# Optimization experiments

Hardware: AMD Instinct MI355X
Metric: run time of the kernel (lower is better)

## Reference

```python
import jax, jax.numpy as jnp
import numpy as np

DIM = 128
HEADS = 8
DIM_HEAD = 128  # must equal DIM for the module's shapes to be consistent
INNER = HEADS * DIM_HEAD  # 1024
B, N = 16, 2048
SCALE = 1.0 / (DIM // 2 + 1)  # 1/65


def setup_inputs() -> dict:
    key = jax.random.key(0)
    k1, k2, k3 = jax.random.split(key, 3)
    x = jax.random.normal(k1, (B, N, DIM), dtype=jnp.float32)
    w_qkv = jax.random.normal(k2, (DIM, 3 * INNER), dtype=jnp.float32) * (DIM ** -0.5)
    w_out = jax.random.normal(k3, (INNER, DIM), dtype=jnp.float32) * (INNER ** -0.5)
    b_out = jnp.zeros((DIM,), dtype=jnp.float32)
    return {"x": x, "w_qkv": w_qkv, "w_out": w_out, "b_out": b_out}


def reference(x, w_qkv, w_out, b_out):
    b, n, dim = x.shape
    qkv = x @ w_qkv                                   # [b, n, 3*inner]
    q, k, v = jnp.split(qkv, 3, axis=-1)
    # b n (h d) -> b h n d
    to_heads = lambda t: t.reshape(b, n, HEADS, DIM_HEAD).transpose(0, 2, 1, 3)
    q, k, v = to_heads(q), to_heads(k), to_heads(v)
    xq_ft = jnp.abs(jnp.fft.rfft(q * SCALE, axis=-1))  # [b, h, n, f] real
    xk_ft = jnp.abs(jnp.fft.rfft(k * SCALE, axis=-1))
    xv_ft = jnp.fft.rfft(v, axis=-1)                   # complex
    att = jnp.einsum('bhex,bhey->bhxy', xq_ft, xk_ft)  # [b, h, f, f]
    att = jax.nn.softmax(att, axis=-1)
    xqkv_ft = jnp.einsum('bhxy,bhey->bhex', att.astype(xv_ft.dtype), xv_ft)
    out = jnp.fft.irfft(xqkv_ft, n=dim, axis=-1)       # [b, h, n, dim]
    out = out.transpose(0, 2, 1, 3).reshape(b, n, HEADS * dim)  # b n (h d)
    return out @ w_out + b_out
```

## Files before the change

kernel.cpp:

```cpp
#include <hip/hip_runtime.h>
#include <hip/hip_bf16.h>
#include <math.h>

#define NB    16
#define NSEQ  2048
#define MROWS (NB*NSEQ)

typedef __attribute__((ext_vector_type(8))) short bf16x8;
typedef __attribute__((ext_vector_type(4))) float f32x4;

__device__ __forceinline__ void g2l16(const void* g, void* l) {
    __builtin_amdgcn_global_load_lds(
        (const __attribute__((address_space(1))) void*)g,
        (__attribute__((address_space(3))) void*)l, 16, 0, 0);
}

__device__ __forceinline__ ushort f2bfu(float x) {
    __hip_bfloat16 t = __float2bfloat16(x);
    return *reinterpret_cast<ushort*>(&t);
}

__global__ __launch_bounds__(256) void k_misc(const float* __restrict__ x,
                                              const float* __restrict__ wqkv,
                                              const float* __restrict__ wout,
                                              __hip_bfloat16* __restrict__ Xb,
                                              ushort* __restrict__ Wvb,
                                              ushort* __restrict__ Wqkb,
                                              ushort* __restrict__ Gcat,
                                              ushort* __restrict__ Fcs,
                                              ushort* __restrict__ Bas) {
    __shared__ float tc[128], ts[128];
    int tid = threadIdx.x;
    int bid = blockIdx.x;
    if (bid < 4096) {
        int i = bid * 256 + tid;
        float4 v = ((const float4*)x)[i];
        __hip_bfloat16 o[4] = {__float2bfloat16(v.x), __float2bfloat16(v.y),
                               __float2bfloat16(v.z), __float2bfloat16(v.w)};
        *(ushort4*)((ushort*)Xb + (size_t)i * 4) = *(const ushort4*)o;
    } else if (bid < 4224) {
        int u = bid - 4096;
        float4 v = *(const float4*)(wqkv + (size_t)u * 3072 + 2048 + tid * 4);
        ushort o[4] = {f2bfu(v.x), f2bfu(v.y), f2bfu(v.z), f2bfu(v.w)};
        *(ushort4*)(Wvb + (size_t)u * 1024 + tid * 4) = *(const ushort4*)o;
    } else if (bid < 4352) {
        int u = bid - 4224;
        #pragma unroll
        for (int it = 0; it < 2; ++it) {
            int i = it * 256 + tid;
            float4 v = ((const float4*)(wqkv + (size_t)u * 3072))[i];
            ushort o[4] = {f2bfu(v.x), f2bfu(v.y), f2bfu(v.z), f2bfu(v.w)};
            *(ushort4*)(Wqkb + (size_t)u * 2048 + i * 4) = *(const ushort4*)o;
        }
    } else if (bid < 4872) {
        int hx = bid - 4352;
        if (tid < 128) {
            float a = (float)tid / 64.0f;
            tc[tid] = cospif(a);
            ts[tid] = sinpif(a);
        }
        __syncthreads();
        if (tid < 128) {
            int h = hx / 65, xx = hx - h * 65;
            float w = (xx == 0 || xx == 64) ? (1.0f / 128.0f) : (2.0f / 128.0f);
            float ar = 0.f, ai = 0.f;
            #pragma unroll 8
            for (int d = 0; d < 128; ++d) {
                float wv = wout[(size_t)(h * 128 + d) * 128 + tid];
                int m = (xx * d) & 127;
                ar = fmaf(wv, tc[m], ar);
                ai = fmaf(wv, ts[m], ai);
            }
            ushort* gp = Gcat + ((size_t)(h * 128 + tid)) * 160;
            gp[xx] = f2bfu(ar * w);
            gp[80 + xx] = f2bfu(-ai * w);
            if (xx == 0) {
                for (int k = 65; k < 80; ++k) gp[k] = 0;
                for (int k = 145; k < 160; ++k) gp[k] = 0;
            }
        }
    } else if (bid < 4888) {
        int r = (bid - 4872) * 16 + (tid >> 4);
        int d = r & 127;
        int y0 = (tid & 15) * 6;
        #pragma unroll
        for (int k = 0; k < 6; ++k) {
            int y = y0 + k;
            float v = 0.f;
            if (y < 65) {
                float a = (float)((d * y) & 127) / 64.0f;
                v = (r < 128) ? cospif(a) : -sinpif(a);
            }
            Fcs[r * 96 + y] = f2bfu(v);
        }
    } else {
        int idx = bid - 4888;
        int rj = idx * 16 + (tid >> 4);
        int ri = (rj >= 80) ? 1 : 0;
        int f = rj - ri * 80;
        int d0 = (tid & 15) * 8;
        #pragma unroll
        for (int k = 0; k < 8; ++k) {
            int d = d0 + k;
            float a = (float)((f * d) & 127) / 64.0f;
            float v = (ri ? -sinpif(a) : cospif(a)) * (1.0f / 65.0f);
            Bas[rj * 128 + d] = f2bfu(v);
        }
    }
}

__global__ __launch_bounds__(256) void k_wfold(const ushort* __restrict__ Wqkb,
                                               const ushort* __restrict__ Bas,
                                               ushort* __restrict__ Wt2) {
    __shared__ ushort As[128 * 128];
    __shared__ ushort Bs[160 * 128];
    int tid = threadIdx.x;
    int wave = tid >> 6, lane = tid & 63;
    int reg = blockIdx.x >> 3, h = blockIdx.x & 7;
    const ushort* ga = Wqkb + reg * 1024 + h * 128;
    #pragma unroll
    for (int it = 0; it < 8; ++it) {
        int q0 = wave * 512 + it * 64;
        int q = q0 + lane;
        int row = q >> 4, cp = q & 15;
        int gc = cp ^ (row & 15);
        g2l16(ga + (size_t)row * 2048 + gc * 8, As + q0 * 8);
    }
    #pragma unroll
    for (int it = 0; it < 10; ++it) {
        int q0 = it * 256 + wave * 64;
        int q = q0 + lane;
        int row = q >> 4, cp = q & 15;
        int gc = cp ^ (row & 15);
        g2l16(Bas + (size_t)row * 128 + gc * 8, Bs + q0 * 8);
    }
    __syncthreads();

    f32x4 acc[4][5];
    #pragma unroll
    for (int i = 0; i < 4; ++i)
        #pragma unroll
        for (int j = 0; j < 5; ++j) acc[i][j] = (f32x4){0.f, 0.f, 0.f, 0.f};

    int lr = lane & 15, lk = lane >> 4;
    int wr = (wave >> 1) * 64;
    int wn = (wave & 1) * 80;
    #pragma unroll
    for (int kk = 0; kk < 4; ++kk) {
        bf16x8 af[4], bfr[5];
        int c = kk * 4 + lk;
        #pragma unroll
        for (int i = 0; i < 4; ++i) {
            int m = wr + i * 16 + lr;
            af[i] = *(const bf16x8*)(As + m * 128 + (c ^ (m & 15)) * 8);
        }
        #pragma unroll
        for (int j = 0; j < 5; ++j) {
            int n = wn + j * 16 + lr;
            bfr[j] = *(const bf16x8*)(Bs + n * 128 + (c ^ (n & 15)) * 8);
        }
        #pragma unroll
        for (int i = 0; i < 4; ++i)
            #pragma unroll
            for (int j = 0; j < 5; ++j)
                acc[i][j] = __builtin_amdgcn_mfma_f32_16x16x32_bf16(af[i], bfr[j], acc[i][j], 0, 0, 0);
    }

    #pragma unroll
    for (int j = 0; j < 5; ++j) {
        int rj = wn + j * 16 + lr;
        int n = (h * 2 + reg) * 160 + rj;
        #pragma unroll
        for (int i = 0; i < 4; ++i) {
            int c0 = wr + i * 16 + lk * 4;
            union { ushort4 u4; ushort u[4]; } pk;
            #pragma unroll
            for (int r = 0; r < 4; ++r) pk.u[r] = f2bfu(acc[i][j][r]);
            *(ushort4*)(Wt2 + (size_t)n * 128 + c0) = pk.u4;
        }
    }
}

__global__ __launch_bounds__(320, 3) void k_fuse(const __hip_bfloat16* __restrict__ Xb,
                                                 const ushort* __restrict__ Wt2,
                                                 float* __restrict__ attp) {
    __shared__ ushort As[128 * 128];
    __shared__ ushort S[160 * 128];
    int tid = threadIdx.x;
    int wave = tid >> 6, lane = tid & 63;
    int lr = lane & 15, lk = lane >> 4;
    int lin = blockIdx.y * 128 + blockIdx.x;
    int nl = (lin & 7) * 64 + (lin >> 3);
    int b = nl >> 5;
    int epart = (nl >> 3) & 3, h = nl & 7;
    size_t erow0 = (size_t)b * NSEQ + (size_t)epart * 512;
    const ushort* wh = Wt2 + (size_t)h * 320 * 128;

    bf16x8 bw[4][4];
    #pragma unroll
    for (int ks = 0; ks < 4; ++ks)
        #pragma unroll
        for (int rb = 0; rb < 4; ++rb) {
            int n = rb * 80 + wave * 16 + lr;
            bw[ks][rb] = *(const bf16x8*)(wh + (size_t)n * 128 + (ks * 4 + lk) * 8);
        }

    {
        const ushort* gx = (const ushort*)Xb + erow0 * 128;
        for (int r = wave; r < 32; r += 5) {
            int q0 = r * 64, q = q0 + lane;
            int row = q >> 4, cp = q & 15;
            int gc = cp ^ (row & 15);
            g2l16(gx + (size_t)row * 128 + gc * 8, As + q0 * 8);
        }
    }
    __syncthreads();

    f32x4 acc2[5];
    #pragma unroll
    for (int j = 0; j < 5; ++j) acc2[j] = (f32x4){0.f, 0.f, 0.f, 0.f};

    for (int it = 0; it < 4; ++it) {
        #pragma unroll
        for (int et = 0; et < 8; ++et) {
            f32x4 a4[4];
            #pragma unroll
            for (int rb = 0; rb < 4; ++rb) a4[rb] = (f32x4){0.f, 0.f, 0.f, 0.f};
            #pragma unroll
            for (int ks = 0; ks < 4; ++ks) {
                int m = et * 16 + lr;
                bf16x8 xa = *(const bf16x8*)(As + m * 128 + (((ks * 4 + lk) ^ (m & 15))) * 8);
                #pragma unroll
                for (int rb = 0; rb < 4; ++rb)
                    a4[rb] = __builtin_amdgcn_mfma_f32_16x16x32_bf16(xa, bw[ks][rb], a4[rb], 0, 0, 0);
            }
            int e4 = et * 16 + lk * 4;
            int cq = e4 >> 3, sub = e4 & 7;
            union { ushort4 u4; ushort u[4]; } pq, pk2;
            #pragma unroll
            for (int r = 0; r < 4; ++r) {
                pq.u[r]  = f2bfu(__builtin_amdgcn_sqrtf(a4[0][r] * a4[0][r] + a4[1][r] * a4[1][r]));
                pk2.u[r] = f2bfu(__builtin_amdgcn_sqrtf(a4[2][r] * a4[2][r] + a4[3][r] * a4[3][r]));
            }
            int fq = wave * 16 + lr;
            int fk = 80 + wave * 16 + lr;
            *(ushort4*)(S + fq * 128 + ((cq ^ (fq & 15)) << 3) + sub) = pq.u4;
            *(ushort4*)(S + fk * 128 + ((cq ^ (fk & 15)) << 3) + sub) = pk2.u4;
        }
        __syncthreads();
        if (it < 3) {
            const ushort* gx = (const ushort*)Xb + (erow0 + (size_t)(it + 1) * 128) * 128;
            for (int r = wave; r < 32; r += 5) {
                int q0 = r * 64, q = q0 + lane;
                int row = q >> 4, cp = q & 15;
                int gc = cp ^ (row & 15);
                g2l16(gx + (size_t)row * 128 + gc * 8, As + q0 * 8);
            }
        }
        #pragma unroll
        for (int ks = 0; ks < 4; ++ks) {
            int cg = ks * 4 + lk;
            int xr = wave * 16 + lr;
            bf16x8 qa = *(const bf16x8*)(S + xr * 128 + ((cg ^ (xr & 15)) << 3));
            #pragma unroll
            for (int kt = 0; kt < 5; ++kt) {
                int yr = 80 + kt * 16 + lr;
                bf16x8 kb = *(const bf16x8*)(S + yr * 128 + ((cg ^ (yr & 15)) << 3));
                acc2[kt] = __builtin_amdgcn_mfma_f32_16x16x32_bf16(qa, kb, acc2[kt], 0, 0, 0);
            }
        }
        __syncthreads();
    }

    float* outp = attp + ((size_t)(b * 8 + h) * 4 + epart) * 6400;
    #pragma unroll
    for (int kt = 0; kt < 5; ++kt)
        #pragma unroll
        for (int r = 0; r < 4; ++r)
            outp[(wave * 16 + lk * 4 + r) * 80 + kt * 16 + lr] = acc2[kt][r];
}

__global__ void k_softmax(const float* __restrict__ attp, ushort* __restrict__ AttB) {
    int xx = blockIdx.x;
    int bh = blockIdx.y;
    int lane = threadIdx.x;
    ushort* Ab = AttB + (size_t)bh * 8320;
    if (xx >= 65) {
        Ab[xx * 104 + lane] = 0;
        if (lane < 40) Ab[xx * 104 + 64 + lane] = 0;
        return;
    }
    const float* base = attp + (size_t)bh * 4 * 6400 + xx * 80;
    float v0 = 0.f, v1 = 0.f;
    #pragma unroll
    for (int c = 0; c < 4; ++c) {
        v0 += base[(size_t)c * 6400 + lane];
        if (lane == 0) v1 += base[(size_t)c * 6400 + 64];
    }
    float v1b = __shfl(v1, 0);
    float m = fmaxf(v0, v1b);
    #pragma unroll
    for (int off = 32; off >= 1; off >>= 1) m = fmaxf(m, __shfl_xor(m, off));
    float e0 = expf(v0 - m);
    float e1 = expf(v1b - m);
    float s = e0;
    #pragma unroll
    for (int off = 32; off >= 1; off >>= 1) s += __shfl_xor(s, off);
    s += e1;
    float inv = 1.0f / s;
    Ab[xx * 104 + lane] = f2bfu(e0 * inv);
    if (lane == 0) Ab[xx * 104 + 64] = f2bfu(e1 * inv);
    if (lane < 39) Ab[xx * 104 + 65 + lane] = 0;
}

__global__ __launch_bounds__(256) void k_TP(const ushort* __restrict__ AttB,
                                            const ushort* __restrict__ Fcs,
                                            const ushort* __restrict__ Gcat,
                                            ushort* __restrict__ Pt) {
    __shared__ ushort A3[128 * 168];
    int tid = threadIdx.x;
    int wave = tid >> 6, lane = tid & 63;
    int lr = lane & 15, quad = lane >> 4;
    int chalf = blockIdx.x, bh = blockIdx.y;
    int b = bh >> 3, h = bh & 7;

    uint2 z2; z2.x = 0; z2.y = 0;
    uint2* A3v = (uint2*)A3;
    #pragma unroll 4
    for (int i = tid; i < 128 * 168 / 4; i += 256) A3v[i] = z2;
    __syncthreads();
    const ushort* Ab = AttB + (size_t)bh * 8320;

    f32x4 acc1[4][5];
    #pragma unroll
    for (int i = 0; i < 4; ++i)
        #pragma unroll
        for (int j = 0; j < 5; ++j) acc1[i][j] = (f32x4){0.f, 0.f, 0.f, 0.f};
    #pragma unroll
    for (int ks = 0; ks < 3; ++ks) {
        bf16x8 af[4], bfr[5];
        #pragma unroll
        for (int mi = 0; mi < 4; ++mi)
            af[mi] = *(const bf16x8*)(Fcs + (size_t)((wave * 4 + mi) * 16 + lr) * 96 + ks * 32 + quad * 8);
        #pragma unroll
        for (int nt = 0; nt < 5; ++nt)
            bfr[nt] = *(const bf16x8*)(Ab + (nt * 16 + lr) * 104 + ks * 32 + quad * 8);
        #pragma unroll
        for (int mi = 0; mi < 4; ++mi)
            #pragma unroll
            for (int nt = 0; nt < 5; ++nt)
                acc1[mi][nt] = __builtin_amdgcn_mfma_f32_16x16x32_bf16(af[mi], bfr[nt], acc1[mi][nt], 0, 0, 0);
    }
    #pragma unroll
    for (int nt = 0; nt < 5; ++nt) {
        int x = nt * 16 + lr;
        if (x < 65) {
            #pragma unroll
            for (int mi = 0; mi < 4; ++mi) {
                int wbase = (wave * 4 + mi) * 16 + quad * 4;
                #pragma unroll
                for (int r = 0; r < 4; ++r) {
                    int which = wbase + r;
                    int d = which & 127;
                    int kc = (which >> 7) * 80 + x;
                    A3[d * 168 + kc] = f2bfu(acc1[mi][nt][r]);
                }
            }
        }
    }
    __syncthreads();

    f32x4 acc2[2][4];
    #pragma unroll
    for (int i = 0; i < 2; ++i)
        #pragma unroll
        for (int j = 0; j < 4; ++j) acc2[i][j] = (f32x4){0.f, 0.f, 0.f, 0.f};
    const ushort* Gh = Gcat + (size_t)h * 128 * 160;
    #pragma unroll
    for (int ks = 0; ks < 5; ++ks) {
        bf16x8 a2[2], b2[4];
        #pragma unroll
        for (int mi = 0; mi < 2; ++mi)
            a2[mi] = *(const bf16x8*)(A3 + ((wave * 2 + mi) * 16 + lr) * 168 + ks * 32 + quad * 8);
        #pragma unroll
        for (int nt = 0; nt < 4; ++nt)
            b2[nt] = *(const bf16x8*)(Gh + (size_t)(chalf * 64 + nt * 16 + lr) * 160 + ks * 32 + quad * 8);
        #pragma unroll
        for (int mi = 0; mi < 2; ++mi)
            #pragma unroll
            for (int nt = 0; nt < 4; ++nt)
                acc2[mi][nt] = __builtin_amdgcn_mfma_f32_16x16x32_bf16(a2[mi], b2[nt], acc2[mi][nt], 0, 0, 0);
    }
    #pragma unroll
    for (int mi = 0; mi < 2; ++mi) {
        int dbase = (wave * 2 + mi) * 16 + quad * 4;
        #pragma unroll
        for (int nt = 0; nt < 4; ++nt) {
            int c = chalf * 64 + nt * 16 + lr;
            union { ushort4 u4; ushort u[4]; } pk;
            #pragma unroll
            for (int r = 0; r < 4; ++r) pk.u[r] = f2bfu(acc2[mi][nt][r]);
            *(ushort4*)(Pt + ((size_t)(b * 128 + c)) * 1024 + h * 128 + dbase) = pk.u4;
        }
    }
}

__global__ __launch_bounds__(256) void k_R(const ushort* __restrict__ Wvb,
                                           const ushort* __restrict__ Pt,
                                           ushort* __restrict__ Rt) {
    __shared__ ushort As[128 * 128];
    __shared__ ushort Bs[128 * 128];
    int tid = threadIdx.x;
    int wave = tid >> 6, lane = tid & 63;
    int b = blockIdx.x;
    const ushort* pb = Pt + (size_t)b * 128 * 1024;

    f32x4 acc[4][4];
    #pragma unroll
    for (int i = 0; i < 4; ++i)
        #pragma unroll
        for (int j = 0; j < 4; ++j) acc[i][j] = (f32x4){0.f, 0.f, 0.f, 0.f};

    int lr = lane & 15, lk = lane >> 4;
    int wr = (wave >> 1) * 64, wc = (wave & 1) * 64;

    for (int k0 = 0; k0 < 1024; k0 += 128) {
        __syncthreads();
        #pragma unroll
        for (int it = 0; it < 8; ++it) {
            int q = wave * 512 + it * 64 + lane;
            int row = q >> 4, cp = q & 15;
            int gc = cp ^ (row & 15);
            int lbase = (wave * 512 + it * 64) * 8;
            g2l16(Wvb + (size_t)row * 1024 + k0 + gc * 8, As + lbase);
            g2l16(pb + (size_t)row * 1024 + k0 + gc * 8, Bs + lbase);
        }
        __syncthreads();
        #pragma unroll
        for (int kk = 0; kk < 4; ++kk) {
            bf16x8 af[4], bfr[4];
            int c = kk * 4 + lk;
            #pragma unroll
            for (int i = 0; i < 4; ++i) {
                int m = wr + i * 16 + lr;
                af[i] = *(const bf16x8*)(As + m * 128 + (c ^ (m & 15)) * 8);
                int n = wc + i * 16 + lr;
                bfr[i] = *(const bf16x8*)(Bs + n * 128 + (c ^ (n & 15)) * 8);
            }
            #pragma unroll
            for (int i = 0; i < 4; ++i)
                #pragma unroll
                for (int j = 0; j < 4; ++j)
                    acc[i][j] = __builtin_amdgcn_mfma_f32_16x16x32_bf16(af[i], bfr[j], acc[i][j], 0, 0, 0);
        }
    }
    #pragma unroll
    for (int i = 0; i < 4; ++i) {
        int ubase = wr + i * 16 + lk * 4;
        #pragma unroll
        for (int j = 0; j < 4; ++j) {
            int n = wc + j * 16 + lr;
            union { ushort4 u4; ushort u[4]; } pk;
            #pragma unroll
            for (int r = 0; r < 4; ++r) pk.u[r] = f2bfu(acc[i][j][r]);
            *(ushort4*)(Rt + (size_t)b * 16384 + n * 128 + ubase) = pk.u4;
        }
    }
}

__global__ __launch_bounds__(256) void k_out(const __hip_bfloat16* __restrict__ Xb,
                                             const ushort* __restrict__ Rt,
                                             const float* __restrict__ bout,
                                             float* __restrict__ out) {
    __shared__ ushort As[128 * 128];
    __shared__ ushort Bs[128 * 128];
    int tid = threadIdx.x;
    int wave = tid >> 6, lane = tid & 63;
    int m0 = blockIdx.x * 128;
    int b = blockIdx.x >> 4;
    const ushort* ga = (const ushort*)Xb + (size_t)m0 * 128;
    const ushort* gb = Rt + (size_t)b * 16384;
    #pragma unroll
    for (int it = 0; it < 8; ++it) {
        int q = wave * 512 + it * 64 + lane;
        int row = q >> 4, cp = q & 15;
        int gc = cp ^ (row & 15);
        int lbase = (wave * 512 + it * 64) * 8;
        g2l16(ga + (size_t)row * 128 + gc * 8, As + lbase);
        g2l16(gb + (size_t)row * 128 + gc * 8, Bs + lbase);
    }
    __syncthreads();

    f32x4 acc[4][4];
    #pragma unroll
    for (int i = 0; i < 4; ++i)
        #pragma unroll
        for (int j = 0; j < 4; ++j) acc[i][j] = (f32x4){0.f, 0.f, 0.f, 0.f};

    int lr = lane & 15, lk = lane >> 4;
    int wr = (wave >> 1) * 64, wc = (wave & 1) * 64;
    #pragma unroll
    for (int kk = 0; kk < 4; ++kk) {
        bf16x8 af[4], bfr[4];
        int c = kk * 4 + lk;
        #pragma unroll
        for (int i = 0; i < 4; ++i) {
            int m = wr + i * 16 + lr;
            af[i] = *(const bf16x8*)(As + m * 128 + (c ^ (m & 15)) * 8);
            int n = wc + i * 16 + lr;
            bfr[i] = *(const bf16x8*)(Bs + n * 128 + (c ^ (n & 15)) * 8);
        }
        #pragma unroll
        for (int i = 0; i < 4; ++i)
            #pragma unroll
            for (int j = 0; j < 4; ++j)
                acc[i][j] = __builtin_amdgcn_mfma_f32_16x16x32_bf16(af[i], bfr[j], acc[i][j], 0, 0, 0);
    }

    #pragma unroll
    for (int i = 0; i < 4; ++i) {
        int gr = m0 + wr + i * 16 + lk * 4;
        #pragma unroll
        for (int j = 0; j < 4; ++j) {
            int gcol = wc + j * 16 + lr;
            float bias = bout[gcol];
            #pragma unroll
            for (int r = 0; r < 4; ++r)
                out[(size_t)(gr + r) * 128 + gcol] = acc[i][j][r] + bias;
        }
    }
}

extern "C" void kernel_launch(void* const* d_in, const int* in_sizes, int n_in,
                              void* d_out, int out_size, void* d_ws, size_t ws_size,
                              hipStream_t stream) {
    const float* x    = (const float*)d_in[0];
    const float* wqkv = (const float*)d_in[1];
    const float* wout = (const float*)d_in[2];
    const float* bout = (const float*)d_in[3];
    float* out = (float*)d_out;

    char* ws = (char*)d_ws;
    size_t off = 0;
    auto alloc = [&](size_t bytes) -> void* {
        void* p = (void*)(ws + off);
        off += (bytes + 255) & ~(size_t)255;
        return p;
    };
    ushort* Wt2  = (ushort*)alloc((size_t)8 * 320 * 128 * 2);
    ushort* Gcat = (ushort*)alloc((size_t)8 * 128 * 160 * 2);
    ushort* Fcs  = (ushort*)alloc((size_t)256 * 96 * 2);
    ushort* Wvb  = (ushort*)alloc((size_t)128 * 1024 * 2);
    ushort* Wqkb = (ushort*)alloc((size_t)128 * 2048 * 2);
    ushort* Bas  = (ushort*)alloc((size_t)160 * 128 * 2);
    __hip_bfloat16* Xb = (__hip_bfloat16*)alloc((size_t)MROWS * 128 * 2);
    float* attp = (float*)alloc((size_t)128 * 4 * 6400 * 4);
    ushort* AttB = (ushort*)alloc((size_t)128 * 8320 * 2);
    ushort* Pt  = (ushort*)alloc((size_t)16 * 128 * 1024 * 2);
    ushort* Rt  = (ushort*)alloc((size_t)16 * 128 * 128 * 2);

    k_misc<<<dim3(4898), 256, 0, stream>>>(x, wqkv, wout, Xb, Wvb, Wqkb, Gcat, Fcs, Bas);
    k_wfold<<<dim3(16), 256, 0, stream>>>(Wqkb, Bas, Wt2);
    k_fuse<<<dim3(128, 4), 320, 0, stream>>>(Xb, Wt2, attp);
    k_softmax<<<dim3(80, 128), 64, 0, stream>>>(attp, AttB);
    k_TP<<<dim3(2, 128), 256, 0, stream>>>(AttB, Fcs, Gcat, Pt);
    k_R<<<dim3(16), 256, 0, stream>>>(Wvb, Pt, Rt);
    k_out<<<dim3(256), 256, 0, stream>>>(Xb, Rt, bout, out);
}
```

Before: 159.1 us.

## Fuse softmax into k_TP and split k_wfold and k_R across more blocks

Removes the separate softmax kernel. k_TP now reduces the four partial attention sums, applies the softmax and writes the bf16 result into shared memory before its matmul, so one launch and the AttB global round trip go away. k_wfold is split over two row halves (32 blocks) and k_R over four output quadrants (64 blocks) to fill more CUs on these tiny grids. The cost is that the softmax work is done twice, once per chalf block, and the k_R blocks reload overlapping operands.

After: 168.1 us. 1.06x slower.

```diff
diff --git a/kernel.cpp b/kernel.cpp
--- a/kernel.cpp
+++ b/kernel.cpp
@@ -112,15 +112,17 @@
 __global__ __launch_bounds__(256) void k_wfold(const ushort* __restrict__ Wqkb,
                                                const ushort* __restrict__ Bas,
                                                ushort* __restrict__ Wt2) {
-    __shared__ ushort As[128 * 128];
+    __shared__ ushort As[64 * 128];
     __shared__ ushort Bs[160 * 128];
     int tid = threadIdx.x;
     int wave = tid >> 6, lane = tid & 63;
-    int reg = blockIdx.x >> 3, h = blockIdx.x & 7;
-    const ushort* ga = Wqkb + reg * 1024 + h * 128;
-    #pragma unroll
-    for (int it = 0; it < 8; ++it) {
-        int q0 = wave * 512 + it * 64;
+    int reg = blockIdx.x >> 4;
+    int h = (blockIdx.x >> 1) & 7;
+    int uh = blockIdx.x & 1;
+    const ushort* ga = Wqkb + (size_t)(uh * 64) * 2048 + reg * 1024 + h * 128;
+    #pragma unroll
+    for (int it = 0; it < 4; ++it) {
+        int q0 = wave * 256 + it * 64;
         int q = q0 + lane;
         int row = q >> 4, cp = q & 15;
         int gc = cp ^ (row & 15);
@@ -136,21 +138,21 @@
     }
     __syncthreads();
 
-    f32x4 acc[4][5];
-    #pragma unroll
-    for (int i = 0; i < 4; ++i)
+    f32x4 acc[2][5];
+    #pragma unroll
+    for (int i = 0; i < 2; ++i)
         #pragma unroll
         for (int j = 0; j < 5; ++j) acc[i][j] = (f32x4){0.f, 0.f, 0.f, 0.f};
 
     int lr = lane & 15, lk = lane >> 4;
-    int wr = (wave >> 1) * 64;
+    int wr = (wave >> 1) * 32;
     int wn = (wave & 1) * 80;
     #pragma unroll
     for (int kk = 0; kk < 4; ++kk) {
-        bf16x8 af[4], bfr[5];
+        bf16x8 af[2], bfr[5];
         int c = kk * 4 + lk;
         #pragma unroll
-        for (int i = 0; i < 4; ++i) {
+        for (int i = 0; i < 2; ++i) {
             int m = wr + i * 16 + lr;
             af[i] = *(const bf16x8*)(As + m * 128 + (c ^ (m & 15)) * 8);
         }
@@ -160,7 +162,7 @@
             bfr[j] = *(const bf16x8*)(Bs + n * 128 + (c ^ (n & 15)) * 8);
         }
         #pragma unroll
-        for (int i = 0; i < 4; ++i)
+        for (int i = 0; i < 2; ++i)
             #pragma unroll
             for (int j = 0; j < 5; ++j)
                 acc[i][j] = __builtin_amdgcn_mfma_f32_16x16x32_bf16(af[i], bfr[j], acc[i][j], 0, 0, 0);
@@ -171,8 +173,8 @@
         int rj = wn + j * 16 + lr;
         int n = (h * 2 + reg) * 160 + rj;
         #pragma unroll
-        for (int i = 0; i < 4; ++i) {
-            int c0 = wr + i * 16 + lk * 4;
+        for (int i = 0; i < 2; ++i) {
+            int c0 = uh * 64 + wr + i * 16 + lk * 4;
             union { ushort4 u4; ushort u[4]; } pk;
             #pragma unroll
             for (int r = 0; r < 4; ++r) pk.u[r] = f2bfu(acc[i][j][r]);
@@ -280,56 +282,53 @@
             outp[(wave * 16 + lk * 4 + r) * 80 + kt * 16 + lr] = acc2[kt][r];
 }
 
-__global__ void k_softmax(const float* __restrict__ attp, ushort* __restrict__ AttB) {
-    int xx = blockIdx.x;
-    int bh = blockIdx.y;
-    int lane = threadIdx.x;
-    ushort* Ab = AttB + (size_t)bh * 8320;
-    if (xx >= 65) {
-        Ab[xx * 104 + lane] = 0;
-        if (lane < 40) Ab[xx * 104 + 64 + lane] = 0;
-        return;
-    }
-    const float* base = attp + (size_t)bh * 4 * 6400 + xx * 80;
-    float v0 = 0.f, v1 = 0.f;
-    #pragma unroll
-    for (int c = 0; c < 4; ++c) {
-        v0 += base[(size_t)c * 6400 + lane];
-        if (lane == 0) v1 += base[(size_t)c * 6400 + 64];
-    }
-    float v1b = __shfl(v1, 0);
-    float m = fmaxf(v0, v1b);
-    #pragma unroll
-    for (int off = 32; off >= 1; off >>= 1) m = fmaxf(m, __shfl_xor(m, off));
-    float e0 = expf(v0 - m);
-    float e1 = expf(v1b - m);
-    float s = e0;
-    #pragma unroll
-    for (int off = 32; off >= 1; off >>= 1) s += __shfl_xor(s, off);
-    s += e1;
-    float inv = 1.0f / s;
-    Ab[xx * 104 + lane] = f2bfu(e0 * inv);
-    if (lane == 0) Ab[xx * 104 + 64] = f2bfu(e1 * inv);
-    if (lane < 39) Ab[xx * 104 + 65 + lane] = 0;
-}
-
-__global__ __launch_bounds__(256) void k_TP(const ushort* __restrict__ AttB,
+__global__ __launch_bounds__(256) void k_TP(const float* __restrict__ attp,
                                             const ushort* __restrict__ Fcs,
                                             const ushort* __restrict__ Gcat,
                                             ushort* __restrict__ Pt) {
     __shared__ ushort A3[128 * 168];
+    __shared__ ushort Ab[80 * 104];
     int tid = threadIdx.x;
     int wave = tid >> 6, lane = tid & 63;
     int lr = lane & 15, quad = lane >> 4;
-    int chalf = blockIdx.x, bh = blockIdx.y;
+    int bh = blockIdx.x, chalf = blockIdx.y;
     int b = bh >> 3, h = bh & 7;
 
     uint2 z2; z2.x = 0; z2.y = 0;
     uint2* A3v = (uint2*)A3;
     #pragma unroll 4
     for (int i = tid; i < 128 * 168 / 4; i += 256) A3v[i] = z2;
+    uint2* Abv = (uint2*)Ab;
+    #pragma unroll 4
+    for (int i = tid; i < 80 * 104 / 4; i += 256) Abv[i] = z2;
     __syncthreads();
-    const ushort* Ab = AttB + (size_t)bh * 8320;
+
+    const float* pbase = attp + (size_t)bh * 4 * 6400;
+    for (int p = 0; p < 17; ++p) {
+        int xx = p * 4 + wave;
+        if (xx < 65) {
+            float v0 = 0.f, v1 = 0.f;
+            #pragma unroll
+            for (int c = 0; c < 4; ++c) {
+                v0 += pbase[(size_t)c * 6400 + xx * 80 + lane];
+                if (lane == 0) v1 += pbase[(size_t)c * 6400 + xx * 80 + 64];
+            }
+            float v1b = __shfl(v1, 0);
+            float m = fmaxf(v0, v1b);
+            #pragma unroll
+            for (int off = 32; off >= 1; off >>= 1) m = fmaxf(m, __shfl_xor(m, off));
+            float e0 = expf(v0 - m);
+            float e1 = expf(v1b - m);
+            float s = e0;
+            #pragma unroll
+            for (int off = 32; off >= 1; off >>= 1) s += __shfl_xor(s, off);
+            s += e1;
+            float inv = 1.0f / s;
+            Ab[xx * 104 + lane] = f2bfu(e0 * inv);
+            if (lane == 0) Ab[xx * 104 + 64] = f2bfu(e1 * inv);
+        }
+    }
+    __syncthreads();
 
     f32x4 acc1[4][5];
     #pragma unroll
@@ -408,58 +407,60 @@
 __global__ __launch_bounds__(256) void k_R(const ushort* __restrict__ Wvb,
                                            const ushort* __restrict__ Pt,
                                            ushort* __restrict__ Rt) {
-    __shared__ ushort As[128 * 128];
-    __shared__ ushort Bs[128 * 128];
+    __shared__ ushort As[64 * 128];
+    __shared__ ushort Bs[64 * 128];
     int tid = threadIdx.x;
     int wave = tid >> 6, lane = tid & 63;
-    int b = blockIdx.x;
+    int b = blockIdx.x >> 2;
+    int nq = (blockIdx.x >> 1) & 1;
+    int uq = blockIdx.x & 1;
     const ushort* pb = Pt + (size_t)b * 128 * 1024;
 
-    f32x4 acc[4][4];
-    #pragma unroll
-    for (int i = 0; i < 4; ++i)
-        #pragma unroll
-        for (int j = 0; j < 4; ++j) acc[i][j] = (f32x4){0.f, 0.f, 0.f, 0.f};
+    f32x4 acc[2][2];
+    #pragma unroll
+    for (int i = 0; i < 2; ++i)
+        #pragma unroll
+        for (int j = 0; j < 2; ++j) acc[i][j] = (f32x4){0.f, 0.f, 0.f, 0.f};
 
     int lr = lane & 15, lk = lane >> 4;
-    int wr = (wave >> 1) * 64, wc = (wave & 1) * 64;
+    int wr = (wave >> 1) * 32, wc = (wave & 1) * 32;
 
     for (int k0 = 0; k0 < 1024; k0 += 128) {
         __syncthreads();
         #pragma unroll
-        for (int it = 0; it < 8; ++it) {
-            int q = wave * 512 + it * 64 + lane;
+        for (int it = 0; it < 4; ++it) {
+            int q = wave * 256 + it * 64 + lane;
             int row = q >> 4, cp = q & 15;
             int gc = cp ^ (row & 15);
-            int lbase = (wave * 512 + it * 64) * 8;
-            g2l16(Wvb + (size_t)row * 1024 + k0 + gc * 8, As + lbase);
-            g2l16(pb + (size_t)row * 1024 + k0 + gc * 8, Bs + lbase);
+            int lbase = (wave * 256 + it * 64) * 8;
+            g2l16(Wvb + (size_t)(uq * 64 + row) * 1024 + k0 + gc * 8, As + lbase);
+            g2l16(pb + (size_t)(nq * 64 + row) * 1024 + k0 + gc * 8, Bs + lbase);
         }
         __syncthreads();
         #pragma unroll
         for (int kk = 0; kk < 4; ++kk) {
-            bf16x8 af[4], bfr[4];
+            bf16x8 af[2], bfr[2];
             int c = kk * 4 + lk;
             #pragma unroll
-            for (int i = 0; i < 4; ++i) {
+            for (int i = 0; i < 2; ++i) {
                 int m = wr + i * 16 + lr;
                 af[i] = *(const bf16x8*)(As + m * 128 + (c ^ (m & 15)) * 8);
                 int n = wc + i * 16 + lr;
                 bfr[i] = *(const bf16x8*)(Bs + n * 128 + (c ^ (n & 15)) * 8);
             }
             #pragma unroll
-            for (int i = 0; i < 4; ++i)
+            for (int i = 0; i < 2; ++i)
                 #pragma unroll
-                for (int j = 0; j < 4; ++j)
+                for (int j = 0; j < 2; ++j)
                     acc[i][j] = __builtin_amdgcn_mfma_f32_16x16x32_bf16(af[i], bfr[j], acc[i][j], 0, 0, 0);
         }
     }
     #pragma unroll
-    for (int i = 0; i < 4; ++i) {
-        int ubase = wr + i * 16 + lk * 4;
-        #pragma unroll
-        for (int j = 0; j < 4; ++j) {
-            int n = wc + j * 16 + lr;
+    for (int i = 0; i < 2; ++i) {
+        int ubase = uq * 64 + wr + i * 16 + lk * 4;
+        #pragma unroll
+        for (int j = 0; j < 2; ++j) {
+            int n = nq * 64 + wc + j * 16 + lr;
             union { ushort4 u4; ushort u[4]; } pk;
             #pragma unroll
             for (int r = 0; r < 4; ++r) pk.u[r] = f2bfu(acc[i][j][r]);
@@ -555,15 +556,13 @@
     ushort* Bas  = (ushort*)alloc((size_t)160 * 128 * 2);
     __hip_bfloat16* Xb = (__hip_bfloat16*)alloc((size_t)MROWS * 128 * 2);
     float* attp = (float*)alloc((size_t)128 * 4 * 6400 * 4);
-    ushort* AttB = (ushort*)alloc((size_t)128 * 8320 * 2);
     ushort* Pt  = (ushort*)alloc((size_t)16 * 128 * 1024 * 2);
     ushort* Rt  = (ushort*)alloc((size_t)16 * 128 * 128 * 2);
 
     k_misc<<<dim3(4898), 256, 0, stream>>>(x, wqkv, wout, Xb, Wvb, Wqkb, Gcat, Fcs, Bas);
-    k_wfold<<<dim3(16), 256, 0, stream>>>(Wqkb, Bas, Wt2);
+    k_wfold<<<dim3(32), 256, 0, stream>>>(Wqkb, Bas, Wt2);
     k_fuse<<<dim3(128, 4), 320, 0, stream>>>(Xb, Wt2, attp);
-    k_softmax<<<dim3(80, 128), 64, 0, stream>>>(attp, AttB);
-    k_TP<<<dim3(2, 128), 256, 0, stream>>>(AttB, Fcs, Gcat, Pt);
-    k_R<<<dim3(16), 256, 0, stream>>>(Wvb, Pt, Rt);
+    k_TP<<<dim3(128, 2), 256, 0, stream>>>(attp, Fcs, Gcat, Pt);
+    k_R<<<dim3(64), 256, 0, stream>>>(Wvb, Pt, Rt);
     k_out<<<dim3(256), 256, 0, stream>>>(Xb, Rt, bout, out);
 }
```
